# Optimization experiments

Measured on AMD Instinct MI355X. Metric: run time of the kernel, lower is better.

## Reference

```python
import jax, jax.numpy as jnp
import numpy as np


def gcn_conv(x, edge_index, W, b):
    n = x.shape[0]
    loop = jnp.arange(n, dtype=edge_index.dtype)
    src = jnp.concatenate([edge_index[0], loop])  # message sources (x_j)
    dst = jnp.concatenate([edge_index[1], loop])  # aggregation targets
    deg = jax.ops.segment_sum(jnp.ones_like(dst, dtype=x.dtype), dst, num_segments=n)
    dinv = jnp.where(deg > 0, jax.lax.rsqrt(deg), 0.0)
    norm = dinv[src] * dinv[dst]                  # [E+n]
    xw = x @ W                                    # transform before gather (n << E)
    msg = xw[src] * norm[:, None]                 # [E+n, H]
    return jax.ops.segment_sum(msg, dst, num_segments=n) + b


def mean_pool(x, batch, num_graphs):
    s = jax.ops.segment_sum(x, batch, num_segments=num_graphs)
    cnt = jax.ops.segment_sum(jnp.ones_like(batch, dtype=x.dtype), batch, num_segments=num_graphs)
    return s / jnp.maximum(cnt, 1.0)[:, None]


def setup_inputs() -> dict:
    key = jax.random.key(0)
    ks = jax.random.split(key, 20)
    G, H = 256, 128
    Np, Ep = 100000, 1600000
    Nl, El = 8192, 65536
    sc = lambda fan_in: 1.0 / np.sqrt(fan_in)
    inp = {
        "protein_x": jax.random.normal(ks[0], (Np, 23), jnp.float32),
        "protein_edge_index": jax.random.randint(ks[1], (2, Ep), 0, Np),
        "protein_batch": jnp.sort(jax.random.randint(ks[2], (Np,), 0, G)),
        "ligand_x": jax.random.normal(ks[3], (Nl, 4), jnp.float32),
        "ligand_edge_index": jax.random.randint(ks[4], (2, El), 0, Nl),
        "ligand_batch": jnp.sort(jax.random.randint(ks[5], (Nl,), 0, G)),
        "num_graphs": G,
        "Wp1": jax.random.normal(ks[6], (23, H), jnp.float32) * sc(23),
        "bp1": jnp.zeros((H,), jnp.float32),
        "Wp2": jax.random.normal(ks[7], (H, H), jnp.float32) * sc(H),
        "bp2": jnp.zeros((H,), jnp.float32),
        "Wl1": jax.random.normal(ks[8], (4, H), jnp.float32) * sc(4),
        "bl1": jnp.zeros((H,), jnp.float32),
        "Wl2": jax.random.normal(ks[9], (H, H), jnp.float32) * sc(H),
        "bl2": jnp.zeros((H,), jnp.float32),
        "Wfc1": jax.random.normal(ks[10], (2 * H, H), jnp.float32) * sc(2 * H),
        "bfc1": jnp.zeros((H,), jnp.float32),
        "Wpkd": jax.random.normal(ks[11], (H, 1), jnp.float32) * sc(H),
        "bpkd": jnp.zeros((1,), jnp.float32),
        "Wpki": jax.random.normal(ks[12], (H, 1), jnp.float32) * sc(H),
        "bpki": jnp.zeros((1,), jnp.float32),
        "Wba": jax.random.normal(ks[13], (H, 1), jnp.float32) * sc(H),
        "bba": jnp.zeros((1,), jnp.float32),
    }
    return inp


def reference(protein_x, protein_edge_index, protein_batch,
              ligand_x, ligand_edge_index, ligand_batch, num_graphs,
              Wp1, bp1, Wp2, bp2, Wl1, bl1, Wl2, bl2,
              Wfc1, bfc1, Wpkd, bpkd, Wpki, bpki, Wba, bba):
    # protein GNN
    hp = jax.nn.relu(gcn_conv(protein_x, protein_edge_index, Wp1, bp1))
    hp = jax.nn.relu(gcn_conv(hp, protein_edge_index, Wp2, bp2))
    protein_emb = mean_pool(hp, protein_batch, num_graphs)
    # ligand GNN
    hl = jax.nn.relu(gcn_conv(ligand_x, ligand_edge_index, Wl1, bl1))
    hl = jax.nn.relu(gcn_conv(hl, ligand_edge_index, Wl2, bl2))
    ligand_emb = mean_pool(hl, ligand_batch, num_graphs)
    combined = jnp.concatenate([protein_emb, ligand_emb], axis=1)  # [G, 2H]
    combined = jax.nn.relu(combined @ Wfc1 + bfc1)
    pkd = combined @ Wpkd + bpkd
    pki = combined @ Wpki + bpki
    ba = combined @ Wba + bba
    return (pkd, pki, ba)
```

## Files before the change

### kernel.cpp

```cpp
#include <hip/hip_runtime.h>


typedef unsigned short ushort_t;
typedef short bf16x8 __attribute__((ext_vector_type(8)));
typedef float f32x4 __attribute__((ext_vector_type(4)));

#define SCAN_CHUNK 2048
#define BSHIFT 8
#define EPB 4096
#define MAXBK 1024

static __device__ inline ushort_t f2bf(float f) {
  unsigned u = __float_as_uint(f);
  unsigned r = (u + 0x7FFFu + ((u >> 16) & 1u)) >> 16;
  return (ushort_t)r;
}
static __device__ inline float bf2f(ushort_t b) {
  return __uint_as_float((unsigned)b << 16);
}
static __device__ inline unsigned pack2bf(float lo, float hi) {
  return (unsigned)f2bf(lo) | ((unsigned)f2bf(hi) << 16);
}

__global__ void count_deg2_kernel(const int* __restrict__ dstP, int Ep, int* __restrict__ degP,
                                  const int* __restrict__ dstL, int El, int* __restrict__ degL) {
  int e = blockIdx.x * blockDim.x + threadIdx.x;
  if (e < Ep) atomicAdd(&degP[dstP[e]], 1);
  else if (e < Ep + El) atomicAdd(&degL[dstL[e - Ep]], 1);
}

__device__ inline void node_prep_dev(const int* deg, float* dinv, const int* batch,
                                     int* start, int i, int n, int G) {
  dinv[i] = rsqrtf((float)(deg[i] + 1));
  int b = batch[i];
  if (i == 0) { for (int g = 0; g <= b; ++g) start[g] = 0; }
  else { int pb = batch[i - 1]; for (int g = pb + 1; g <= b; ++g) start[g] = i; }
  if (i == n - 1) { for (int g = b + 1; g <= G; ++g) start[g] = n; }
}

__global__ void node_prep_kernel(const int* __restrict__ degP, float* __restrict__ dinvP,
                                 const int* __restrict__ batchP, int* __restrict__ startP, int nP,
                                 const int* __restrict__ degL, float* __restrict__ dinvL,
                                 const int* __restrict__ batchL, int* __restrict__ startL, int nL,
                                 int G) {
  int i = blockIdx.x * blockDim.x + threadIdx.x;
  if (i < nP) node_prep_dev(degP, dinvP, batchP, startP, i, nP, G);
  int j = i - nP;
  if (j >= 0 && j < nL) node_prep_dev(degL, dinvL, batchL, startL, j, nL, G);
}

__global__ void wprep_kernel(const float* __restrict__ Wp2, ushort_t* __restrict__ WtP,
                             const float* __restrict__ Wl2, ushort_t* __restrict__ WtL,
                             const float* __restrict__ px, unsigned* __restrict__ xbfP, int Np) {
  int i = blockIdx.x * blockDim.x + threadIdx.x;
  if (i < 16384) {
    int f = i >> 7, k = i & 127;
    WtP[i] = f2bf(Wp2[k * 128 + f]);
  } else if (i < 32768) {
    int j = i - 16384;
    int f = j >> 7, k = j & 127;
    WtL[j] = f2bf(Wl2[k * 128 + f]);
  } else {
    int j = i - 32768;
    if (j < Np * 16) {
      int row = j >> 4, c2 = (j & 15) * 2;
      float lo = (c2     < 23) ? px[(size_t)row * 23 + c2]     : 0.f;
      float hi = (c2 + 1 < 23) ? px[(size_t)row * 23 + c2 + 1] : 0.f;
      xbfP[j] = pack2bf(lo, hi);
    }
  }
}

__device__ inline void blocksum_dev(const int* cnt, int* bsum, int n, int b) {
  int t = threadIdx.x;
  int base = b * SCAN_CHUNK;
  int s = 0;
  for (int i = t; i < SCAN_CHUNK; i += 256) {
    int idx = base + i;
    if (idx < n) s += cnt[idx];
  }
  #pragma unroll
  for (int d = 32; d; d >>= 1) s += __shfl_down(s, d, 64);
  __shared__ int wt[4];
  int lane = t & 63, wid = t >> 6;
  if (lane == 0) wt[wid] = s;
  __syncthreads();
  if (t == 0) bsum[b] = wt[0] + wt[1] + wt[2] + wt[3];
}

__global__ __launch_bounds__(256) void blocksum2_kernel(
    const int* __restrict__ cntP, int nP, int nbP, int* __restrict__ bsumP,
    const int* __restrict__ cntL, int nL, int* __restrict__ bsumL) {
  int b = blockIdx.x;
  if (b < nbP) blocksum_dev(cntP, bsumP, nP, b);
  else blocksum_dev(cntL, bsumL, nL, b - nbP);
}

__device__ inline void exscan_small_dev(const int* bsum, int* boffs, int nb) {
  int t = threadIdx.x;
  int v = (t < nb) ? bsum[t] : 0;
  int lane = t & 63, wid = t >> 6;
  int inc = v;
  #pragma unroll
  for (int d = 1; d < 64; d <<= 1) {
    int u = __shfl_up(inc, d, 64);
    if (lane >= d) inc += u;
  }
  __shared__ int wt[16];
  if (lane == 63) wt[wid] = inc;
  __syncthreads();
  if (t < 16) {
    int w = wt[t];
    #pragma unroll
    for (int d = 1; d < 16; d <<= 1) {
      int u = __shfl_up(w, d, 64);
      if (t >= d) w += u;
    }
    wt[t] = w;
  }
  __syncthreads();
  int excl = (wid ? wt[wid - 1] : 0) + inc - v;
  if (t < nb) boffs[t] = excl;
  if (t == 0) boffs[nb] = wt[15];
}

__global__ __launch_bounds__(1024) void exscan2_kernel(const int* __restrict__ bsumP,
                                                       int* __restrict__ boffsP, int nbP,
                                                       const int* __restrict__ bsumL,
                                                       int* __restrict__ boffsL, int nbL) {
  if (blockIdx.x == 0) exscan_small_dev(bsumP, boffsP, nbP);
  else exscan_small_dev(bsumL, boffsL, nbL);
}

__device__ inline void scan_apply_dev(const int* cnt, const int* boffs, int* offs,
                                      int n, int nb, int b) {
  int t = threadIdx.x;
  int base = b * SCAN_CHUNK + t * 8;
  int v[8];
  int s = 0;
  #pragma unroll
  for (int j = 0; j < 8; ++j) {
    int idx = base + j;
    v[j] = (idx < n) ? cnt[idx] : 0;
    s += v[j];
  }
  int lane = t & 63, wid = t >> 6;
  int inc = s;
  #pragma unroll
  for (int d = 1; d < 64; d <<= 1) {
    int u = __shfl_up(inc, d, 64);
    if (lane >= d) inc += u;
  }
  __shared__ int wt[4];
  if (lane == 63) wt[wid] = inc;
  __syncthreads();
  int wadd = 0;
  for (int w = 0; w < wid; ++w) wadd += wt[w];
  int excl = boffs[b] + wadd + inc - s;
  #pragma unroll
  for (int j = 0; j < 8; ++j) {
    int idx = base + j;
    if (idx < n) offs[idx] = excl;
    excl += v[j];
  }
  if (b == 0 && t == 0) offs[n] = boffs[nb];
}

__global__ __launch_bounds__(256) void scan_apply2_kernel(
    const int* __restrict__ cntP, const int* __restrict__ boffsP, int* __restrict__ offsP,
    int nP, int nbP,
    const int* __restrict__ cntL, const int* __restrict__ boffsL, int* __restrict__ offsL,
    int nL, int nbL) {
  int b = blockIdx.x;
  if (b < nbP) scan_apply_dev(cntP, boffsP, offsP, nP, nbP, b);
  else scan_apply_dev(cntL, boffsL, offsL, nL, nbL, b - nbP);
}

__global__ __launch_bounds__(256) void bin_count_kernel(
    const int* __restrict__ dstP, int Ep, int nbkP, int nbeP, int* __restrict__ cntP,
    const int* __restrict__ dstL, int El, int nbkL, int* __restrict__ cntL) {
  __shared__ int hist[MAXBK];
  int j = blockIdx.x;
  const int* dst; int E, nbk; int* cnt;
  if (j < nbeP) { dst = dstP; E = Ep; nbk = nbkP; cnt = cntP; }
  else { j -= nbeP; dst = dstL; E = El; nbk = nbkL; cnt = cntL; }
  for (int i = threadIdx.x; i < nbk; i += 256) hist[i] = 0;
  __syncthreads();
  int e0 = j * EPB;
  for (int i = threadIdx.x; i < EPB; i += 256) {
    int e = e0 + i;
    if (e < E) atomicAdd(&hist[dst[e] >> BSHIFT], 1);
  }
  __syncthreads();
  for (int i = threadIdx.x; i < nbk; i += 256) cnt[(size_t)j * nbk + i] = hist[i];
}

__global__ __launch_bounds__(256) void bin_scan_kernel(
    const int* __restrict__ offsP, int nbkP, int nbeP, int* __restrict__ mP,
    const int* __restrict__ offsL, int nbkL, int nbeL, int* __restrict__ mL) {
  int b = blockIdx.x;
  const int* offs; int nbk, nbe; int* m;
  if (b < nbkP) { offs = offsP; nbk = nbkP; nbe = nbeP; m = mP; }
  else { b -= nbkP; offs = offsL; nbk = nbkL; nbe = nbeL; m = mL; }
  int t = threadIdx.x, lane = t & 63, wid = t >> 6;
  int j0 = 2 * t;
  int v0 = (j0     < nbe) ? m[(size_t)j0       * nbk + b] : 0;
  int v1 = (j0 + 1 < nbe) ? m[(size_t)(j0 + 1) * nbk + b] : 0;
  int s = v0 + v1;
  int inc = s;
  #pragma unroll
  for (int d = 1; d < 64; d <<= 1) {
    int u = __shfl_up(inc, d, 64);
    if (lane >= d) inc += u;
  }
  __shared__ int wt[4];
  if (lane == 63) wt[wid] = inc;
  __syncthreads();
  int wadd = 0;
  for (int w = 0; w < wid; ++w) wadd += wt[w];
  int excl = offs[b << BSHIFT] + wadd + inc - s;
  if (j0     < nbe) m[(size_t)j0       * nbk + b] = excl;
  if (j0 + 1 < nbe) m[(size_t)(j0 + 1) * nbk + b] = excl + v0;
}

__global__ __launch_bounds__(256) void bin_place_kernel(
    const int* __restrict__ srcP, const int* __restrict__ dstP, int Ep, int nbkP, int nbeP,
    const int* __restrict__ baseP, int2* __restrict__ pairP,
    const int* __restrict__ srcL, const int* __restrict__ dstL, int El, int nbkL,
    const int* __restrict__ baseL, int2* __restrict__ pairL) {
  __shared__ int lbase[MAXBK];
  int j = blockIdx.x;
  const int* src; const int* dst; int E, nbk; const int* base_m; int2* pair;
  if (j < nbeP) { src = srcP; dst = dstP; E = Ep; nbk = nbkP; base_m = baseP; pair = pairP; }
  else { j -= nbeP; src = srcL; dst = dstL; E = El; nbk = nbkL; base_m = baseL; pair = pairL; }
  for (int i = threadIdx.x; i < nbk; i += 256)
    lbase[i] = base_m[(size_t)j * nbk + i];
  __syncthreads();
  int e0 = j * EPB;
  for (int i = threadIdx.x; i < EPB; i += 256) {
    int e = e0 + i;
    if (e < E) {
      int s = src[e], d = dst[e];
      int pos = atomicAdd(&lbase[d >> BSHIFT], 1);
      pair[pos] = make_int2(s, d);
    }
  }
}

__global__ __launch_bounds__(256) void bucket_pass2_kernel(
    const int2* __restrict__ pairP, const int* __restrict__ offsP, int* __restrict__ curP,
    int* __restrict__ ssrcP, int nP, int nbkP,
    const int2* __restrict__ pairL, const int* __restrict__ offsL, int* __restrict__ curL,
    int* __restrict__ ssrcL, int nL) {
  int b = blockIdx.x;
  const int2* pair; const int* offs; int* cur; int* ssrc; int n;
  if (b < nbkP) { pair = pairP; offs = offsP; cur = curP; ssrc = ssrcP; n = nP; }
  else { b -= nbkP; pair = pairL; offs = offsL; cur = curL; ssrc = ssrcL; n = nL; }
  int lo = b << BSHIFT;
  int hi = lo + (1 << BSHIFT); if (hi > n) hi = n;
  int ebeg = offs[lo], eend = offs[hi];
  for (int i = ebeg + threadIdx.x; i < eend; i += 256) {
    int2 p = pair[i];
    int pos = offs[p.y] + atomicAdd(&cur[p.y], 1);
    ssrc[pos] = p.x;
  }
}

__device__ inline void agg1t_bf_dev(const unsigned* __restrict__ x, const int* __restrict__ ssrc,
                                    const int* __restrict__ offs, const float* __restrict__ dinv,
                                    const float2* __restrict__ wp, const float2* __restrict__ bp,
                                    ushort_t* __restrict__ out, int node, int n) {
  if (node >= n) return;
  int lane = threadIdx.x & 63;
  int g = lane >> 4, l = lane & 15;
  int beg = offs[node], end = offs[node + 1];
  float a0 = 0.f, a1 = 0.f;
  for (int b0 = beg; b0 < end; b0 += 64) {
    int m = end - b0; if (m > 64) m = 64;
    int sl = 0; float wl = 0.f;
    if (lane < m) { sl = ssrc[b0 + lane]; wl = dinv[sl]; }
    for (int k = 0; k < m; k += 4) {
      int idx = k + g;
      int s = __shfl(sl, idx, 64);
      float w = __shfl(wl, idx, 64);
      unsigned u = x[(size_t)s * 16 + l];
      a0 += bf2f((ushort_t)(u & 0xffff)) * w;
      a1 += bf2f((ushort_t)(u >> 16)) * w;
    }
  }
  a0 += __shfl_xor(a0, 16, 64); a0 += __shfl_xor(a0, 32, 64);
  a1 += __shfl_xor(a1, 16, 64); a1 += __shfl_xor(a1, 32, 64);
  float di = dinv[node];
  unsigned u = x[(size_t)node * 16 + l];
  a0 = (a0 + bf2f((ushort_t)(u & 0xffff)) * di) * di;
  a1 = (a1 + bf2f((ushort_t)(u >> 16)) * di) * di;
  float2 b2 = bp[lane];
  float s0 = b2.x, s1 = b2.y;
  #pragma unroll
  for (int k = 0; k < 23; ++k) {
    float ak = __shfl((k & 1) ? a1 : a0, k >> 1, 64);
    float2 w2 = wp[k * 64 + lane];
    s0 += ak * w2.x;
    s1 += ak * w2.y;
  }
  out[(size_t)node * 128 + lane]      = f2bf(fmaxf(s0, 0.f) * di);
  out[(size_t)node * 128 + 64 + lane] = f2bf(fmaxf(s1, 0.f) * di);
}

template<int F, int LPG>
__device__ inline void agg1t_dev(const float* __restrict__ x, const int* __restrict__ ssrc,
                                 const int* __restrict__ offs, const float* __restrict__ dinv,
                                 const float2* __restrict__ wp, const float2* __restrict__ bp,
                                 ushort_t* __restrict__ out, int node, int n) {
  if (node >= n) return;
  constexpr int G = 64 / LPG;
  int lane = threadIdx.x & 63;
  int grp = lane / LPG, l = lane % LPG;
  int beg = offs[node], end = offs[node + 1];
  float acc = 0.f;
  for (int b0 = beg; b0 < end; b0 += 64) {
    int m = end - b0; if (m > 64) m = 64;
    int sl = 0; float wl = 0.f;
    if (lane < m) { sl = ssrc[b0 + lane]; wl = dinv[sl]; }
    for (int k = 0; k < m; k += G) {
      int idx = k + grp;
      int s = __shfl(sl, idx, 64);
      float w = __shfl(wl, idx, 64);
      if (l < F) acc += x[(size_t)s * F + l] * w;
    }
  }
  #pragma unroll
  for (int d = LPG; d < 64; d <<= 1) acc += __shfl_xor(acc, d, 64);
  float di = dinv[node];
  if (l < F) acc = (acc + x[(size_t)node * F + l] * di) * di;
  float2 b2 = bp[lane];
  float s0 = b2.x, s1 = b2.y;
  #pragma unroll
  for (int k = 0; k < F; ++k) {
    float ak = __shfl(acc, k, 64);
    float2 w2 = wp[k * 64 + lane];
    s0 += ak * w2.x;
    s1 += ak * w2.y;
  }
  out[(size_t)node * 128 + lane]      = f2bf(fmaxf(s0, 0.f) * di);
  out[(size_t)node * 128 + 64 + lane] = f2bf(fmaxf(s1, 0.f) * di);
}

__global__ __launch_bounds__(256) void agg1t_both_kernel(
    const unsigned* __restrict__ xbfP, const int* __restrict__ ssrcP,
    const int* __restrict__ offsP, const float* __restrict__ dinvP,
    const float* __restrict__ W1P, const float* __restrict__ b1P,
    ushort_t* __restrict__ outP, int nP, int nblkP,
    const float* __restrict__ xL, const int* __restrict__ ssrcL,
    const int* __restrict__ offsL, const float* __restrict__ dinvL,
    const float* __restrict__ W1L, const float* __restrict__ b1L,
    ushort_t* __restrict__ outL, int nL) {
  __shared__ float2 wp[23 * 64];
  __shared__ float2 bp[64];
  const int t = threadIdx.x;
  const int wv = t >> 6;
  const bool isP = (int)blockIdx.x < nblkP;
  const float* W1 = isP ? W1P : W1L;
  const float* b1 = isP ? b1P : b1L;
  const int F = isP ? 23 : 4;
  for (int i = t; i < F * 64; i += 256) {
    int k = i >> 6, l = i & 63;
    wp[i] = make_float2(W1[k * 128 + l], W1[k * 128 + 64 + l]);
  }
  if (t < 64) bp[t] = make_float2(b1[t], b1[t + 64]);
  __syncthreads();
  if (isP) {
    int node0 = (blockIdx.x * 4 + wv) * 4;
    #pragma unroll
    for (int i = 0; i < 4; ++i)
      agg1t_bf_dev(xbfP, ssrcP, offsP, dinvP, wp, bp, outP, node0 + i, nP);
  } else {
    int node0 = ((blockIdx.x - nblkP) * 4 + wv) * 4;
    #pragma unroll
    for (int i = 0; i < 4; ++i)
      agg1t_dev<4, 4>(xL, ssrcL, offsL, dinvL, wp, bp, outL, node0 + i, nL);
  }
}

__device__ inline void agg128v_dev(const ushort_t* __restrict__ x, const int* __restrict__ ssrc,
                                   const int* __restrict__ offs, const float* __restrict__ dinv,
                                   ushort_t* __restrict__ out, int node, int n) {
  if (node >= n) return;
  int lane = threadIdx.x & 63;
  int g = lane >> 4, l = lane & 15;
  int beg = offs[node], end = offs[node + 1];
  float acc[8];
  #pragma unroll
  for (int j = 0; j < 8; ++j) acc[j] = 0.f;
  const uint4* x4 = (const uint4*)x;
  for (int b0 = beg; b0 < end; b0 += 64) {
    int m = end - b0; if (m > 64) m = 64;
    int sl = 0;
    if (lane < m) sl = ssrc[b0 + lane];
    for (int k = 0; k < m; k += 4) {
      int s = __shfl(sl, k + g, 64);
      if (k + g < m) {
        uint4 v = x4[(size_t)s * 16 + l];
        acc[0] += bf2f((ushort_t)(v.x & 0xffff)); acc[1] += bf2f((ushort_t)(v.x >> 16));
        acc[2] += bf2f((ushort_t)(v.y & 0xffff)); acc[3] += bf2f((ushort_t)(v.y >> 16));
        acc[4] += bf2f((ushort_t)(v.z & 0xffff)); acc[5] += bf2f((ushort_t)(v.z >> 16));
        acc[6] += bf2f((ushort_t)(v.w & 0xffff)); acc[7] += bf2f((ushort_t)(v.w >> 16));
      }
    }
  }
  #pragma unroll
  for (int j = 0; j < 8; ++j) {
    acc[j] += __shfl_xor(acc[j], 16, 64);
    acc[j] += __shfl_xor(acc[j], 32, 64);
  }
  if (g == 0) {
    uint4 v = x4[(size_t)node * 16 + l];
    float di = dinv[node];
    float r0 = (acc[0] + bf2f((ushort_t)(v.x & 0xffff))) * di;
    float r1 = (acc[1] + bf2f((ushort_t)(v.x >> 16)))   * di;
    float r2 = (acc[2] + bf2f((ushort_t)(v.y & 0xffff))) * di;
    float r3 = (acc[3] + bf2f((ushort_t)(v.y >> 16)))   * di;
    float r4 = (acc[4] + bf2f((ushort_t)(v.z & 0xffff))) * di;
    float r5 = (acc[5] + bf2f((ushort_t)(v.z >> 16)))   * di;
    float r6 = (acc[6] + bf2f((ushort_t)(v.w & 0xffff))) * di;
    float r7 = (acc[7] + bf2f((ushort_t)(v.w >> 16)))   * di;
    uint4 o;
    o.x = pack2bf(r0, r1); o.y = pack2bf(r2, r3);
    o.z = pack2bf(r4, r5); o.w = pack2bf(r6, r7);
    ((uint4*)out)[(size_t)node * 16 + l] = o;
  }
}

__global__ void agg2_both_kernel(const ushort_t* __restrict__ xP, const int* __restrict__ ssrcP,
                                 const int* __restrict__ offsP, const float* __restrict__ dinvP,
                                 ushort_t* __restrict__ outP, int nP, int nblkP,
                                 const ushort_t* __restrict__ xL, const int* __restrict__ ssrcL,
                                 const int* __restrict__ offsL, const float* __restrict__ dinvL,
                                 ushort_t* __restrict__ outL, int nL) {
  int wv = threadIdx.x >> 6;
  if ((int)blockIdx.x < nblkP)
    agg128v_dev(xP, ssrcP, offsP, dinvP, outP, blockIdx.x * 4 + wv, nP);
  else
    agg128v_dev(xL, ssrcL, offsL, dinvL, outL, (blockIdx.x - nblkP) * 4 + wv, nL);
}

__global__ __launch_bounds__(512) void t2_mfma_kernel(
    const ushort_t* __restrict__ aggP, const ushort_t* __restrict__ WtP,
    const float* __restrict__ bP, float* __restrict__ h2P, int nP, int nblkP,
    const ushort_t* __restrict__ aggL, const ushort_t* __restrict__ WtL,
    const float* __restrict__ bL, float* __restrict__ h2L, int nL) {
  const ushort_t* agg; const ushort_t* Wt; const float* bias; float* out; int n, n0;
  if ((int)blockIdx.x < nblkP) {
    agg = aggP; Wt = WtP; bias = bP; out = h2P; n = nP; n0 = blockIdx.x * 128;
  } else {
    agg = aggL; Wt = WtL; bias = bL; out = h2L; n = nL;
    n0 = (blockIdx.x - nblkP) * 128;
  }
  __shared__ __align__(16) short sB[16384];
  const int t = threadIdx.x;
  const int lane = t & 63;
  const int ws = t >> 6;

  #pragma unroll
  for (int c4 = 0; c4 < 4; ++c4) {
    int cidx = t + c4 * 512;
    int node = cidx >> 4, c = cidx & 15;
    uint4 v = make_uint4(0u, 0u, 0u, 0u);
    if (n0 + node < n) v = *(const uint4*)&agg[(size_t)(n0 + node) * 128 + c * 8];
    int off16 = (((node >> 4) * 4 + (c >> 2)) * 64) + (c & 3) * 16 + (node & 15);
    *(uint4*)&sB[off16 * 8] = v;
  }

  const int fs = ws * 16;
  bf16x8 a[4];
  #pragma unroll
  for (int kc = 0; kc < 4; ++kc)
    a[kc] = *(const bf16x8*)&Wt[(size_t)(fs + (lane & 15)) * 128 + kc * 32 + (lane >> 4) * 8];

  __syncthreads();

  f32x4 acc[8];
  #pragma unroll
  for (int g = 0; g < 8; ++g) acc[g] = (f32x4){0.f, 0.f, 0.f, 0.f};

  #pragma unroll
  for (int g = 0; g < 8; ++g) {
    #pragma unroll
    for (int kc = 0; kc < 4; ++kc) {
      bf16x8 b = *(const bf16x8*)&sB[(((g * 4 + kc) * 64) + lane) * 8];
      acc[g] = __builtin_amdgcn_mfma_f32_16x16x32_bf16(a[kc], b, acc[g], 0, 0, 0);
    }
  }

  const int f0 = fs + ((lane >> 4) << 2);
  float4 bv = *(const float4*)&bias[f0];
  #pragma unroll
  for (int g = 0; g < 8; ++g) {
    int node = n0 + g * 16 + (lane & 15);
    if (node < n) {
      float4 o;
      o.x = fmaxf(acc[g][0] + bv.x, 0.f);
      o.y = fmaxf(acc[g][1] + bv.y, 0.f);
      o.z = fmaxf(acc[g][2] + bv.z, 0.f);
      o.w = fmaxf(acc[g][3] + bv.w, 0.f);
      *(float4*)&out[(size_t)node * 128 + f0] = o;
    }
  }
}

__device__ inline void pool_dev(const float* __restrict__ h, const int* __restrict__ start,
                                float* __restrict__ mean, int g) {
  int t = threadIdx.x;
  int f = t & 127, r = t >> 7;
  int beg = start[g], end = start[g + 1];
  float acc = 0.f;
  for (int i = beg + r; i < end; i += 4)
    acc += h[(size_t)i * 128 + f];
  __shared__ float red[4][128];
  red[r][f] = acc;
  __syncthreads();
  if (r == 0) {
    float s = red[0][f] + red[1][f] + red[2][f] + red[3][f];
    float c = (float)(end - beg);
    mean[(size_t)g * 128 + f] = s / fmaxf(c, 1.f);
  }
}

__global__ __launch_bounds__(512) void pool_both_kernel(
    const float* __restrict__ hP, const int* __restrict__ startP, float* __restrict__ meanP,
    const float* __restrict__ hL, const int* __restrict__ startL, float* __restrict__ meanL,
    int G) {
  int g = blockIdx.x;
  if (g < G) pool_dev(hP, startP, meanP, g);
  else pool_dev(hL, startL, meanL, g - G);
}

__global__ __launch_bounds__(128) void fc_heads_kernel(
    const float* __restrict__ pe, const float* __restrict__ le,
    const float* __restrict__ Wfc, const float* __restrict__ bfc,
    const float* __restrict__ Wpkd, const float* __restrict__ bpkd,
    const float* __restrict__ Wpki, const float* __restrict__ bpki,
    const float* __restrict__ Wba, const float* __restrict__ bba,
    float* __restrict__ out, int G) {
  int g = blockIdx.x, f = threadIdx.x;
  __shared__ float comb[256];
  __shared__ float cbuf[128];
  comb[f]       = pe[(size_t)g * 128 + f];
  comb[128 + f] = le[(size_t)g * 128 + f];
  __syncthreads();
  float acc = bfc[f];
  for (int k = 0; k < 256; ++k) acc += comb[k] * Wfc[(size_t)k * 128 + f];
  cbuf[f] = fmaxf(acc, 0.f);
  __syncthreads();
  if (f < 64) {
    const float* Wh[3] = {Wpkd, Wpki, Wba};
    const float* bh[3] = {bpkd, bpki, bba};
    #pragma unroll
    for (int hd = 0; hd < 3; ++hd) {
      float v = cbuf[f] * Wh[hd][f] + cbuf[f + 64] * Wh[hd][f + 64];
      #pragma unroll
      for (int d = 32; d; d >>= 1) v += __shfl_xor(v, d, 64);
      if (f == 0) out[(size_t)hd * G + g] = v + bh[hd][0];
    }
  }
}

static inline size_t alignUp(size_t x, size_t a) { return (x + a - 1) / a * a; }

extern "C" void kernel_launch(void* const* d_in, const int* in_sizes, int n_in,
                              void* d_out, int out_size, void* d_ws, size_t ws_size,
                              hipStream_t stream) {
  const float* px     = (const float*)d_in[0];
  const int*   pei    = (const int*)d_in[1];
  const int*   pbatch = (const int*)d_in[2];
  const float* lx     = (const float*)d_in[3];
  const int*   lei    = (const int*)d_in[4];
  const int*   lbatch = (const int*)d_in[5];
  const float* Wp1 = (const float*)d_in[7],  *bp1 = (const float*)d_in[8];
  const float* Wp2 = (const float*)d_in[9],  *bp2 = (const float*)d_in[10];
  const float* Wl1 = (const float*)d_in[11], *bl1 = (const float*)d_in[12];
  const float* Wl2 = (const float*)d_in[13], *bl2 = (const float*)d_in[14];
  const float* Wfc = (const float*)d_in[15], *bfc = (const float*)d_in[16];
  const float* Wpkd = (const float*)d_in[17], *bpkd = (const float*)d_in[18];
  const float* Wpki = (const float*)d_in[19], *bpki = (const float*)d_in[20];
  const float* Wba  = (const float*)d_in[21], *bba  = (const float*)d_in[22];
  float* out = (float*)d_out;

  const int Np = in_sizes[0] / 23, Ep = in_sizes[1] / 2;
  const int Nl = in_sizes[3] / 4,  El = in_sizes[4] / 2;
  const int G  = out_size / 3;
  const int nb_p = (Np + SCAN_CHUNK - 1) / SCAN_CHUNK;
  const int nb_l = (Nl + SCAN_CHUNK - 1) / SCAN_CHUNK;
  const int nbk_p = (Np + (1 << BSHIFT) - 1) >> BSHIFT;
  const int nbk_l = (Nl + (1 << BSHIFT) - 1) >> BSHIFT;
  const int nbe_p = (Ep + EPB - 1) / EPB;
  const int nbe_l = (El + EPB - 1) / EPB;

  char* base = (char*)d_ws;
  size_t off = 0;
  auto alloc = [&](size_t bytes) -> void* {
    void* p = base + off;
    off = alignUp(off + bytes, 256);
    return p;
  };
  size_t zero_beg = off;
  int*   degcnt_p = (int*)alloc((size_t)Np * 4);
  int*   cursor_p = (int*)alloc((size_t)Np * 4);
  int*   degcnt_l = (int*)alloc((size_t)Nl * 4);
  int*   cursor_l = (int*)alloc((size_t)Nl * 4);
  size_t zero_end = off;
  int*   offs_p  = (int*)alloc((size_t)(Np + 1) * 4);
  int*   offs_l  = (int*)alloc((size_t)(Nl + 1) * 4);
  int*   bsum_p  = (int*)alloc((size_t)nb_p * 4);
  int*   boffs_p = (int*)alloc((size_t)(nb_p + 1) * 4);
  int*   bsum_l  = (int*)alloc((size_t)nb_l * 4);
  int*   boffs_l = (int*)alloc((size_t)(nb_l + 1) * 4);
  int*   start_p = (int*)alloc((size_t)(G + 1) * 4);
  int*   start_l = (int*)alloc((size_t)(G + 1) * 4);
  float* dinv_p  = (float*)alloc((size_t)Np * 4);
  float* dinv_l  = (float*)alloc((size_t)Nl * 4);
  int*   ssrc_p  = (int*)alloc((size_t)Ep * 4);
  int*   ssrc_l  = (int*)alloc((size_t)El * 4);
  int2*  pair_p  = (int2*)alloc((size_t)Ep * 8);
  int2*  pair_l  = (int2*)alloc((size_t)El * 8);
  int*   cmat_p  = (int*)alloc((size_t)nbe_p * nbk_p * 4);
  int*   cmat_l  = (int*)alloc((size_t)nbe_l * nbk_l * 4);
  float* pe_mean = (float*)alloc((size_t)G * 128 * 4);
  float* le_mean = (float*)alloc((size_t)G * 128 * 4);
  ushort_t* wt2_p = (ushort_t*)alloc((size_t)16384 * 2);
  ushort_t* wt2_l = (ushort_t*)alloc((size_t)16384 * 2);
  unsigned* xbf_p = (unsigned*)alloc((size_t)Np * 16 * 4);
  ushort_t* h1_p   = (ushort_t*)alloc((size_t)Np * 128 * 2);
  ushort_t* agg2_p = (ushort_t*)alloc((size_t)Np * 128 * 2);
  float*    h2_p   = (float*)alloc((size_t)Np * 128 * 4);
  ushort_t* h1_l   = (ushort_t*)alloc((size_t)Nl * 128 * 2);
  ushort_t* agg2_l = (ushort_t*)alloc((size_t)Nl * 128 * 2);
  float*    h2_l   = (float*)alloc((size_t)Nl * 128 * 4);
  if (off > ws_size) return;

  hipMemsetAsync(base + zero_beg, 0, zero_end - zero_beg, stream);

  const int* psrc = pei;
  const int* pdst = pei + Ep;
  const int* lsrc = lei;
  const int* ldst = lei + El;

  wprep_kernel<<<(32768 + Np * 16 + 255) / 256, 256, 0, stream>>>(
      Wp2, wt2_p, Wl2, wt2_l, px, xbf_p, Np);

  count_deg2_kernel<<<(Ep + El + 255) / 256, 256, 0, stream>>>(pdst, Ep, degcnt_p,
                                                               ldst, El, degcnt_l);
  node_prep_kernel<<<(Np + Nl + 255) / 256, 256, 0, stream>>>(
      degcnt_p, dinv_p, pbatch, start_p, Np,
      degcnt_l, dinv_l, lbatch, start_l, Nl, G);
  blocksum2_kernel<<<nb_p + nb_l, 256, 0, stream>>>(degcnt_p, Np, nb_p, bsum_p,
                                                    degcnt_l, Nl, bsum_l);
  exscan2_kernel<<<2, 1024, 0, stream>>>(bsum_p, boffs_p, nb_p, bsum_l, boffs_l, nb_l);
  scan_apply2_kernel<<<nb_p + nb_l, 256, 0, stream>>>(degcnt_p, boffs_p, offs_p, Np, nb_p,
                                                      degcnt_l, boffs_l, offs_l, Nl, nb_l);

  bin_count_kernel<<<nbe_p + nbe_l, 256, 0, stream>>>(
      pdst, Ep, nbk_p, nbe_p, cmat_p,
      ldst, El, nbk_l, cmat_l);
  bin_scan_kernel<<<nbk_p + nbk_l, 256, 0, stream>>>(
      offs_p, nbk_p, nbe_p, cmat_p,
      offs_l, nbk_l, nbe_l, cmat_l);
  bin_place_kernel<<<nbe_p + nbe_l, 256, 0, stream>>>(
      psrc, pdst, Ep, nbk_p, nbe_p, cmat_p, pair_p,
      lsrc, ldst, El, nbk_l, cmat_l, pair_l);
  bucket_pass2_kernel<<<nbk_p + nbk_l, 256, 0, stream>>>(
      pair_p, offs_p, cursor_p, ssrc_p, Np, nbk_p,
      pair_l, offs_l, cursor_l, ssrc_l, Nl);

  const int a1blkP = (Np + 15) / 16, a1blkL = (Nl + 15) / 16;
  agg1t_both_kernel<<<a1blkP + a1blkL, 256, 0, stream>>>(
      xbf_p, ssrc_p, offs_p, dinv_p, Wp1, bp1, h1_p, Np, a1blkP,
      lx, ssrc_l, offs_l, dinv_l, Wl1, bl1, h1_l, Nl);

  const int ablkP = (Np + 3) / 4, ablkL = (Nl + 3) / 4;
  agg2_both_kernel<<<ablkP + ablkL, 256, 0, stream>>>(
      h1_p, ssrc_p, offs_p, dinv_p, agg2_p, Np, ablkP,
      h1_l, ssrc_l, offs_l, dinv_l, agg2_l, Nl);
  const int mblkP = (Np + 127) / 128, mblkL = (Nl + 127) / 128;
  t2_mfma_kernel<<<mblkP + mblkL, 512, 0, stream>>>(
      agg2_p, wt2_p, bp2, h2_p, Np, mblkP,
      agg2_l, wt2_l, bl2, h2_l, Nl);

  pool_both_kernel<<<2 * G, 512, 0, stream>>>(h2_p, start_p, pe_mean,
                                              h2_l, start_l, le_mean, G);
  fc_heads_kernel<<<G, 128, 0, stream>>>(pe_mean, le_mean, Wfc, bfc,
                                         Wpkd, bpkd, Wpki, bpki, Wba, bba, out, G);
}
```

Measured before the change: 342.5 us.

## Pre-scale layer-1 features by dinv and drop shuffle-staged neighbor index loads

Source features are multiplied by their D^-1/2 factor in a new prep kernel that runs after the degree computation. The first-layer aggregation therefore no longer gathers dinv[src] for each edge. All three aggregation loops also drop the batched load-then-shuffle staging of neighbor indices and instead load ssrc directly per lane group. This removes a dependent random gather and the shuffles, but it adds one extra launch and makes each lane group issue its own index loads.

Result: slower. 357.5 us (median of 2 runs) (+4.4%).

```diff
diff --git a/kernel.cpp b/kernel.cpp
--- a/kernel.cpp
+++ b/kernel.cpp
@@ -50,8 +50,7 @@
 }
 
 __global__ void wprep_kernel(const float* __restrict__ Wp2, ushort_t* __restrict__ WtP,
-                             const float* __restrict__ Wl2, ushort_t* __restrict__ WtL,
-                             const float* __restrict__ px, unsigned* __restrict__ xbfP, int Np) {
+                             const float* __restrict__ Wl2, ushort_t* __restrict__ WtL) {
   int i = blockIdx.x * blockDim.x + threadIdx.x;
   if (i < 16384) {
     int f = i >> 7, k = i & 127;
@@ -60,13 +59,25 @@
     int j = i - 16384;
     int f = j >> 7, k = j & 127;
     WtL[j] = f2bf(Wl2[k * 128 + f]);
+  }
+}
+
+__global__ void xprep_kernel(const float* __restrict__ px, const float* __restrict__ dinvP,
+                             unsigned* __restrict__ xbfP, int Np,
+                             const float* __restrict__ lx, const float* __restrict__ dinvL,
+                             float* __restrict__ xlL, int Nl) {
+  int i = blockIdx.x * blockDim.x + threadIdx.x;
+  if (i < Np * 16) {
+    int row = i >> 4, c2 = (i & 15) * 2;
+    float di = dinvP[row];
+    float lo = (c2     < 23) ? px[(size_t)row * 23 + c2]     * di : 0.f;
+    float hi = (c2 + 1 < 23) ? px[(size_t)row * 23 + c2 + 1] * di : 0.f;
+    xbfP[i] = pack2bf(lo, hi);
   } else {
-    int j = i - 32768;
-    if (j < Np * 16) {
-      int row = j >> 4, c2 = (j & 15) * 2;
-      float lo = (c2     < 23) ? px[(size_t)row * 23 + c2]     : 0.f;
-      float hi = (c2 + 1 < 23) ? px[(size_t)row * 23 + c2 + 1] : 0.f;
-      xbfP[j] = pack2bf(lo, hi);
+    int j = i - Np * 16;
+    if (j < Nl * 4) {
+      int row = j >> 2;
+      xlL[j] = lx[j] * dinvL[row];
     }
   }
 }
@@ -275,25 +286,21 @@
   int g = lane >> 4, l = lane & 15;
   int beg = offs[node], end = offs[node + 1];
   float a0 = 0.f, a1 = 0.f;
-  for (int b0 = beg; b0 < end; b0 += 64) {
-    int m = end - b0; if (m > 64) m = 64;
-    int sl = 0; float wl = 0.f;
-    if (lane < m) { sl = ssrc[b0 + lane]; wl = dinv[sl]; }
-    for (int k = 0; k < m; k += 4) {
-      int idx = k + g;
-      int s = __shfl(sl, idx, 64);
-      float w = __shfl(wl, idx, 64);
+  for (int k = beg; k < end; k += 4) {
+    int idx = k + g;
+    if (idx < end) {
+      int s = ssrc[idx];
       unsigned u = x[(size_t)s * 16 + l];
-      a0 += bf2f((ushort_t)(u & 0xffff)) * w;
-      a1 += bf2f((ushort_t)(u >> 16)) * w;
+      a0 += bf2f((ushort_t)(u & 0xffff));
+      a1 += bf2f((ushort_t)(u >> 16));
     }
   }
   a0 += __shfl_xor(a0, 16, 64); a0 += __shfl_xor(a0, 32, 64);
   a1 += __shfl_xor(a1, 16, 64); a1 += __shfl_xor(a1, 32, 64);
   float di = dinv[node];
   unsigned u = x[(size_t)node * 16 + l];
-  a0 = (a0 + bf2f((ushort_t)(u & 0xffff)) * di) * di;
-  a1 = (a1 + bf2f((ushort_t)(u >> 16)) * di) * di;
+  a0 = (a0 + bf2f((ushort_t)(u & 0xffff))) * di;
+  a1 = (a1 + bf2f((ushort_t)(u >> 16))) * di;
   float2 b2 = bp[lane];
   float s0 = b2.x, s1 = b2.y;
   #pragma unroll
@@ -318,21 +325,17 @@
   int grp = lane / LPG, l = lane % LPG;
   int beg = offs[node], end = offs[node + 1];
   float acc = 0.f;
-  for (int b0 = beg; b0 < end; b0 += 64) {
-    int m = end - b0; if (m > 64) m = 64;
-    int sl = 0; float wl = 0.f;
-    if (lane < m) { sl = ssrc[b0 + lane]; wl = dinv[sl]; }
-    for (int k = 0; k < m; k += G) {
-      int idx = k + grp;
-      int s = __shfl(sl, idx, 64);
-      float w = __shfl(wl, idx, 64);
-      if (l < F) acc += x[(size_t)s * F + l] * w;
+  for (int k = beg; k < end; k += G) {
+    int idx = k + grp;
+    if (idx < end && l < F) {
+      int s = ssrc[idx];
+      acc += x[(size_t)s * F + l];
     }
   }
   #pragma unroll
   for (int d = LPG; d < 64; d <<= 1) acc += __shfl_xor(acc, d, 64);
   float di = dinv[node];
-  if (l < F) acc = (acc + x[(size_t)node * F + l] * di) * di;
+  if (l < F) acc = (acc + x[(size_t)node * F + l]) * di;
   float2 b2 = bp[lane];
   float s0 = b2.x, s1 = b2.y;
   #pragma unroll
@@ -351,7 +354,7 @@
     const int* __restrict__ offsP, const float* __restrict__ dinvP,
     const float* __restrict__ W1P, const float* __restrict__ b1P,
     ushort_t* __restrict__ outP, int nP, int nblkP,
-    const float* __restrict__ xL, const int* __restrict__ ssrcL,
+    const float* __restrict__ xlL, const int* __restrict__ ssrcL,
     const int* __restrict__ offsL, const float* __restrict__ dinvL,
     const float* __restrict__ W1L, const float* __restrict__ b1L,
     ushort_t* __restrict__ outL, int nL) {
@@ -378,7 +381,7 @@
     int node0 = ((blockIdx.x - nblkP) * 4 + wv) * 4;
     #pragma unroll
     for (int i = 0; i < 4; ++i)
-      agg1t_dev<4, 4>(xL, ssrcL, offsL, dinvL, wp, bp, outL, node0 + i, nL);
+      agg1t_dev<4, 4>(xlL, ssrcL, offsL, dinvL, wp, bp, outL, node0 + i, nL);
   }
 }
 
@@ -393,19 +396,15 @@
   #pragma unroll
   for (int j = 0; j < 8; ++j) acc[j] = 0.f;
   const uint4* x4 = (const uint4*)x;
-  for (int b0 = beg; b0 < end; b0 += 64) {
-    int m = end - b0; if (m > 64) m = 64;
-    int sl = 0;
-    if (lane < m) sl = ssrc[b0 + lane];
-    for (int k = 0; k < m; k += 4) {
-      int s = __shfl(sl, k + g, 64);
-      if (k + g < m) {
-        uint4 v = x4[(size_t)s * 16 + l];
-        acc[0] += bf2f((ushort_t)(v.x & 0xffff)); acc[1] += bf2f((ushort_t)(v.x >> 16));
-        acc[2] += bf2f((ushort_t)(v.y & 0xffff)); acc[3] += bf2f((ushort_t)(v.y >> 16));
-        acc[4] += bf2f((ushort_t)(v.z & 0xffff)); acc[5] += bf2f((ushort_t)(v.z >> 16));
-        acc[6] += bf2f((ushort_t)(v.w & 0xffff)); acc[7] += bf2f((ushort_t)(v.w >> 16));
-      }
+  for (int k = beg; k < end; k += 4) {
+    int idx = k + g;
+    if (idx < end) {
+      int s = ssrc[idx];
+      uint4 v = x4[(size_t)s * 16 + l];
+      acc[0] += bf2f((ushort_t)(v.x & 0xffff)); acc[1] += bf2f((ushort_t)(v.x >> 16));
+      acc[2] += bf2f((ushort_t)(v.y & 0xffff)); acc[3] += bf2f((ushort_t)(v.y >> 16));
+      acc[4] += bf2f((ushort_t)(v.z & 0xffff)); acc[5] += bf2f((ushort_t)(v.z >> 16));
+      acc[6] += bf2f((ushort_t)(v.w & 0xffff)); acc[7] += bf2f((ushort_t)(v.w >> 16));
     }
   }
   #pragma unroll
@@ -630,6 +629,7 @@
   ushort_t* wt2_p = (ushort_t*)alloc((size_t)16384 * 2);
   ushort_t* wt2_l = (ushort_t*)alloc((size_t)16384 * 2);
   unsigned* xbf_p = (unsigned*)alloc((size_t)Np * 16 * 4);
+  float*    xl_l  = (float*)alloc((size_t)Nl * 4 * 4);
   ushort_t* h1_p   = (ushort_t*)alloc((size_t)Np * 128 * 2);
   ushort_t* agg2_p = (ushort_t*)alloc((size_t)Np * 128 * 2);
   float*    h2_p   = (float*)alloc((size_t)Np * 128 * 4);
@@ -645,14 +645,15 @@
   const int* lsrc = lei;
   const int* ldst = lei + El;
 
-  wprep_kernel<<<(32768 + Np * 16 + 255) / 256, 256, 0, stream>>>(
-      Wp2, wt2_p, Wl2, wt2_l, px, xbf_p, Np);
+  wprep_kernel<<<128, 256, 0, stream>>>(Wp2, wt2_p, Wl2, wt2_l);
 
   count_deg2_kernel<<<(Ep + El + 255) / 256, 256, 0, stream>>>(pdst, Ep, degcnt_p,
                                                                ldst, El, degcnt_l);
   node_prep_kernel<<<(Np + Nl + 255) / 256, 256, 0, stream>>>(
       degcnt_p, dinv_p, pbatch, start_p, Np,
       degcnt_l, dinv_l, lbatch, start_l, Nl, G);
+  xprep_kernel<<<(Np * 16 + Nl * 4 + 255) / 256, 256, 0, stream>>>(
+      px, dinv_p, xbf_p, Np, lx, dinv_l, xl_l, Nl);
   blocksum2_kernel<<<nb_p + nb_l, 256, 0, stream>>>(degcnt_p, Np, nb_p, bsum_p,
                                                     degcnt_l, Nl, bsum_l);
   exscan2_kernel<<<2, 1024, 0, stream>>>(bsum_p, boffs_p, nb_p, bsum_l, boffs_l, nb_l);
@@ -675,7 +676,7 @@
   const int a1blkP = (Np + 15) / 16, a1blkL = (Nl + 15) / 16;
   agg1t_both_kernel<<<a1blkP + a1blkL, 256, 0, stream>>>(
       xbf_p, ssrc_p, offs_p, dinv_p, Wp1, bp1, h1_p, Np, a1blkP,
-      lx, ssrc_l, offs_l, dinv_l, Wl1, bl1, h1_l, Nl);
+      xl_l, ssrc_l, offs_l, dinv_l, Wl1, bl1, h1_l, Nl);
 
   const int ablkP = (Np + 3) / 4, ablkL = (Nl + 3) / 4;
   agg2_both_kernel<<<ablkP + ablkL, 256, 0, stream>>>(
```
